# Performance work log

Hardware: AMD Instinct MI355X
Metric: run time of the kernel (lower is better)

Reference implementation:

```python
import jax, jax.numpy as jnp
import numpy as np


def setup_inputs() -> dict:
    key = jax.random.key(0)
    ks = jax.random.split(key, 5)
    B, T, E, C = 4, 1024, 4, 512
    IN, OUT = 2048, 8192
    return {
        "x": jax.random.normal(ks[0], (B, T, IN), dtype=jnp.float32),
        "combine_array": jax.random.uniform(ks[1], (B, T, E, C), dtype=jnp.float32),
        "dispatch_mask": jax.random.uniform(ks[2], (B, T, E, C), dtype=jnp.float32),
        "weight": jax.random.normal(ks[3], (OUT, IN), dtype=jnp.float32) * 0.02,
        "bias": jax.random.normal(ks[4], (OUT,), dtype=jnp.float32) * 0.02,
        "num_experts": E,
    }


def reference(x, combine_array, dispatch_mask, weight, bias, num_experts):
    E = num_experts
    i = weight.shape[1] // E  # expert_in_features
    w = weight.reshape(E, -1, i)  # (E, out, i) -- same reshape as torch
    B = x.shape[0]
    xr = x.reshape(B, -1, E, i)  # (B, T, E, i)
    # dispatch: gather tokens into expert capacity slots via dense mask
    xd = jnp.einsum('btei,btec->beci', xr, dispatch_mask)  # (B, E, C, i)
    # homogeneous coordinates to fold bias into the matmul (as in original)
    x_homo = jnp.concatenate([xd, jnp.ones_like(xd[..., :1])], axis=-1)  # (B,E,C,i+1)
    b_col = jnp.broadcast_to(bias.reshape(1, -1, 1), (E, w.shape[1], 1))
    w_homo = jnp.concatenate([w, b_col], axis=-1)  # (E, out, i+1)
    # per-expert matmul then combine back to tokens
    y = jnp.einsum('beci,eoi->beco', x_homo, w_homo)  # (B, E, C, out)
    return jnp.einsum('beco,btec->bto', y, combine_array)  # (B, T, out)
```

## Files before the change

### kernel.cpp

```cpp
#include <hip/hip_runtime.h>

#define B_   4
#define T_   1024
#define E_   4
#define C_   512
#define IN_  2048
#define OUT_ 8192
#define EI_  512

typedef float f32x4 __attribute__((ext_vector_type(4)));
typedef __bf16 bf16x8 __attribute__((ext_vector_type(8)));
typedef unsigned short ushort8 __attribute__((ext_vector_type(8)));

__device__ __forceinline__ unsigned short f32_bf16(float f) {
  unsigned int u = __float_as_uint(f);
  u += 0x7FFFu + ((u >> 16) & 1u);
  return (unsigned short)(u >> 16);
}

__device__ __forceinline__ void gl2lds16(const void* g, void* l) {
  __builtin_amdgcn_global_load_lds(
      (const __attribute__((address_space(1))) void*)g,
      (__attribute__((address_space(3))) void*)l, 16, 0, 0);
}

__global__ __launch_bounds__(256)
void prep(const float* __restrict__ xsrc, const float* __restrict__ msrc,
          const float* __restrict__ combine, const float* __restrict__ weight,
          unsigned short* __restrict__ xdst, unsigned short* __restrict__ mdst,
          unsigned short* __restrict__ comb_bf, float* __restrict__ S,
          unsigned short* __restrict__ W2) {
  const int bid = blockIdx.x;
  const int u = threadIdx.x;
  if (bid < 4096) {
    __shared__ float tile[64][65];
    const int z = bid >> 9;
    const int which = z >> 2;
    const int b = z & 3;
    const int rem = bid & 511;
    const int t0 = (rem >> 5) * 64;
    const int k0 = (rem & 31) * 64;
    const float* src = which ? msrc : xsrc;
    unsigned short* dst = which ? mdst : xdst;
    const int lrow = u >> 4;
    const int lcol = (u & 15) * 4;
    const float* s = src + (size_t)b * (T_ * 2048) + (size_t)t0 * 2048 + k0;
#pragma unroll
    for (int r = 0; r < 4; r++) {
      float4 v = *(const float4*)(s + (size_t)(lrow + 16 * r) * 2048 + lcol);
      tile[lrow + 16 * r][lcol]     = v.x;
      tile[lrow + 16 * r][lcol + 1] = v.y;
      tile[lrow + 16 * r][lcol + 2] = v.z;
      tile[lrow + 16 * r][lcol + 3] = v.w;
    }
    __syncthreads();
    const int kr = u >> 2;
    const int tq = (u & 3) * 8;
    const int kg = k0 + kr;
    const int e  = kg >> 9;
    const int kl = kg & 511;
    unsigned short* d = dst + (((size_t)b * 4 + e) * 512 + kl) * 1024 + t0 + tq;
#pragma unroll
    for (int s8 = 0; s8 < 2; s8++) {
      ushort8 rr;
#pragma unroll
      for (int j = 0; j < 8; j++) rr[j] = f32_bf16(tile[tq + s8 * 32 + j][kr]);
      *(ushort8*)(d + s8 * 32) = rr;
    }
  } else if (bid < 8192) {
    __shared__ float red[256];
    const int row = bid - 4096;
    const float4* p = (const float4*)(combine + (size_t)row * 2048) + (size_t)u * 2;
    float4 a = p[0], b = p[1];
    ushort8 r;
    r[0] = f32_bf16(a.x); r[1] = f32_bf16(a.y);
    r[2] = f32_bf16(a.z); r[3] = f32_bf16(a.w);
    r[4] = f32_bf16(b.x); r[5] = f32_bf16(b.y);
    r[6] = f32_bf16(b.z); r[7] = f32_bf16(b.w);
    *((ushort8*)(comb_bf + (size_t)row * 2048) + u) = r;
    float s = (a.x + a.y + a.z + a.w) + (b.x + b.y + b.z + b.w);
    red[u] = s;
    __syncthreads();
#pragma unroll
    for (int st = 128; st > 0; st >>= 1) {
      if (u < st) red[u] += red[u + st];
      __syncthreads();
    }
    if (u == 0) S[row] = red[0];
  } else {
    const int tid = (bid - 8192) * 256 + u;
    const int i8 = tid & 63;
    const int e  = (tid >> 6) & 3;
    const int o  = tid >> 8;
    const float* s = weight + (size_t)e * 4194304 + (size_t)o * 512 + i8 * 8;
    float4 a = *(const float4*)s;
    float4 b = *(const float4*)(s + 4);
    ushort8 r;
    r[0] = f32_bf16(a.x); r[1] = f32_bf16(a.y);
    r[2] = f32_bf16(a.z); r[3] = f32_bf16(a.w);
    r[4] = f32_bf16(b.x); r[5] = f32_bf16(b.y);
    r[6] = f32_bf16(b.z); r[7] = f32_bf16(b.w);
    *(ushort8*)(W2 + (size_t)o * 2048 + e * 512 + i8 * 8) = r;
  }
}

template <int MODE>
__global__ __launch_bounds__(256, 2)
void gemm_bt(const unsigned short* __restrict__ A,
             const unsigned short* __restrict__ Bm,
             void* __restrict__ Out, const float* __restrict__ bias,
             const float* __restrict__ S,
             int lda, int ldb, int ldo, int K, int Ediv,
             long sAb, long sAe, long sBb, long sBe, long sOb, long sOe) {
  __shared__ __align__(16) unsigned short As[2][4096];
  __shared__ __align__(16) unsigned short Bs[2][4096];
  const int u = threadIdx.x;
  const int z = blockIdx.z;
  const int zb = z / Ediv, ze = z % Ediv;
  const unsigned short* Ab = A  + zb * sAb + ze * sAe + (long)(blockIdx.y * 128) * lda;
  const unsigned short* Bb = Bm + zb * sBb + ze * sBe + (long)(blockIdx.x * 128) * ldb;

  const int srow = u >> 2;
  const int scol = (u & 3) * 8;
  const unsigned short* ga0 = Ab + (long)srow * lda + scol;
  const unsigned short* ga1 = ga0 + (long)64 * lda;
  const unsigned short* gb0 = Bb + (long)srow * ldb + scol;
  const unsigned short* gb1 = gb0 + (long)64 * ldb;

  const int w = u >> 6, lane = u & 63;
  const int wq = w * 512;

  const int wm = (w & 1) * 64, wn = (w >> 1) * 64;
  const int fm = lane & 15, fk = (lane >> 4) * 8;

  f32x4 acc[4][4] = {};

  gl2lds16(ga0, As[0] + wq);
  gl2lds16(ga1, As[0] + wq + 2048);
  gl2lds16(gb0, Bs[0] + wq);
  gl2lds16(gb1, Bs[0] + wq + 2048);
  ga0 += 32; ga1 += 32; gb0 += 32; gb1 += 32;
  __syncthreads();

  const int nt = K / 32;
  for (int t = 0; t < nt; ++t) {
    const int cur = t & 1;
    if (t + 1 < nt) {
      const int nx = cur ^ 1;
      gl2lds16(ga0, As[nx] + wq);
      gl2lds16(ga1, As[nx] + wq + 2048);
      gl2lds16(gb0, Bs[nx] + wq);
      gl2lds16(gb1, Bs[nx] + wq + 2048);
      ga0 += 32; ga1 += 32; gb0 += 32; gb1 += 32;
    }
    const unsigned short* pA = As[cur] + (wm + fm) * 32 + fk;
    const unsigned short* pB = Bs[cur] + (wn + fm) * 32 + fk;
    bf16x8 af[4], bfv[4];
#pragma unroll
    for (int i = 0; i < 4; i++) {
      af[i]  = *(const bf16x8*)(pA + i * 16 * 32);
      bfv[i] = *(const bf16x8*)(pB + i * 16 * 32);
    }
#pragma unroll
    for (int i = 0; i < 4; i++)
#pragma unroll
      for (int j = 0; j < 4; j++)
        acc[i][j] = __builtin_amdgcn_mfma_f32_16x16x32_bf16(af[i], bfv[j],
                                                            acc[i][j], 0, 0, 0);
    __syncthreads();
  }

  const long ob = zb * sOb + ze * sOe;
  const int em0 = blockIdx.y * 128 + wm + ((lane >> 4) << 2);
  const int en0 = blockIdx.x * 128 + wn + (lane & 15);
  float bcol[4];
  if (MODE == 1) {
#pragma unroll
    for (int j = 0; j < 4; j++) bcol[j] = bias[en0 + j * 16];
  }
#pragma unroll
  for (int i = 0; i < 4; i++)
#pragma unroll
    for (int r = 0; r < 4; r++) {
      const int m = em0 + i * 16 + r;
      const float sm = (MODE == 1) ? S[m] : 0.0f;
#pragma unroll
      for (int j = 0; j < 4; j++) {
        const long off = ob + (long)m * ldo + en0 + j * 16;
        if (MODE == 1)
          ((float*)Out)[off] = acc[i][j][r] + sm * bcol[j];
        else
          ((unsigned short*)Out)[off] = f32_bf16(acc[i][j][r]);
      }
    }
}

#define DSR(dst, addr) do { f32x4 _t_; \
    asm volatile("ds_read_b128 %0, %1" : "=v"(_t_) : "v"(addr)); \
    dst = __builtin_bit_cast(bf16x8, _t_); } while (0)

__global__ __launch_bounds__(512, 2)
void gemm256(const unsigned short* __restrict__ A,
             const unsigned short* __restrict__ Bm,
             float* __restrict__ Out,
             const float* __restrict__ bias,
             const float* __restrict__ S) {
  __shared__ __align__(16) unsigned short lds[65536];
  char* ldsg = (char*)lds;
  const unsigned ldsb =
      (unsigned)(unsigned long long)(__attribute__((address_space(3))) char*)(void*)lds;

  int wg = blockIdx.x;
  wg = (wg & 7) * 64 + (wg >> 3);
  const int bx = wg & 31;
  const int by = wg >> 5;

  const int u = threadIdx.x;
  const int w = u >> 6, lane = u & 63;
  const unsigned w1024 = (unsigned)(w * 1024);
  const int wmw = (w >> 2) * 128;
  const int wnw = (w & 3) * 64;
  const int fm = lane & 15;

  const unsigned hi16  = (unsigned)(((lane >> 4) & 3) * 16);
  const unsigned xorv  = (unsigned)((fm & 7) << 4);
  const unsigned colS0 = hi16 ^ xorv;
  const unsigned aR0 = (unsigned)((wmw + fm) * 128) + colS0;
  const unsigned aR1 = aR0 ^ 64u;
  const unsigned bR0 = 65536u + (unsigned)((wnw + fm) * 128) + colS0;
  const unsigned bR1 = bR0 ^ 64u;

  const int srr = w * 8 + (lane >> 3);
  const unsigned swzS = (unsigned)((((lane & 7) ^ ((lane >> 3) & 7)) << 4));
  const char* gA = (const char*)(A  + (size_t)(by * 256) * 2048) + (size_t)srr * 4096 + swzS;
  const char* gB = (const char*)(Bm + (size_t)(bx * 256) * 2048) + (size_t)srr * 4096 + swzS;

#define STG(gsrc, loff) do { \
    gl2lds16((gsrc), ldsg + (loff)); \
    gl2lds16((gsrc) + 262144, ldsg + (loff) + 8192); } while (0)

  STG(gA,                    0u + w1024);
  STG(gA + 524288,       16384u + w1024);
  STG(gB,                65536u + w1024);
  STG(gB + 524288,       81920u + w1024);
  STG(gA + 128,          32768u + w1024);
  STG(gA + 128 + 524288, 49152u + w1024);
  asm volatile("s_waitcnt vmcnt(4)" ::: "memory");
  __builtin_amdgcn_s_barrier();

  f32x4 acc[8][4] = {};
  bf16x8 a0[4][2], a1[4][2], bq[2][2];

  for (int kt = 0; kt < 32; ++kt) {
    const unsigned bbO = (unsigned)((kt & 1) * 32768);
    const unsigned nbR = bbO ^ 32768u;
    const int ktB = (kt + 1 < 32) ? kt + 1 : 31;
    const int ktA = (kt + 2 < 32) ? kt + 2 : 31;
    const char* gBn = gB + ktB * 128;
    const char* gAn = gA + ktA * 128;

#pragma unroll
    for (int i = 0; i < 4; ++i) {
      DSR(a0[i][0], ldsb + bbO + aR0 + (unsigned)(i * 2048));
      DSR(a0[i][1], ldsb + bbO + aR1 + (unsigned)(i * 2048));
    }
#pragma unroll
    for (int j = 0; j < 2; ++j) {
      DSR(bq[j][0], ldsb + bbO + bR0 + (unsigned)(j * 2048));
      DSR(bq[j][1], ldsb + bbO + bR1 + (unsigned)(j * 2048));
    }
    STG(gBn, 65536u + nbR + w1024);
    __builtin_amdgcn_s_barrier();
    asm volatile("s_waitcnt lgkmcnt(0)" ::: "memory");
    __builtin_amdgcn_sched_barrier(0);
    __builtin_amdgcn_s_setprio(1);
#pragma unroll
    for (int i = 0; i < 4; ++i)
#pragma unroll
      for (int j = 0; j < 2; ++j) {
        acc[i][j] = __builtin_amdgcn_mfma_f32_16x16x32_bf16(a0[i][0], bq[j][0], acc[i][j], 0, 0, 0);
        acc[i][j] = __builtin_amdgcn_mfma_f32_16x16x32_bf16(a0[i][1], bq[j][1], acc[i][j], 0, 0, 0);
      }
    __builtin_amdgcn_s_setprio(0);
    __builtin_amdgcn_s_barrier();

#pragma unroll
    for (int i = 0; i < 4; ++i) {
      DSR(a1[i][0], ldsb + bbO + aR0 + (unsigned)((4 + i) * 2048));
      DSR(a1[i][1], ldsb + bbO + aR1 + (unsigned)((4 + i) * 2048));
    }
    STG(gBn + 524288, 81920u + nbR + w1024);
    __builtin_amdgcn_s_barrier();
    asm volatile("s_waitcnt lgkmcnt(0)" ::: "memory");
    __builtin_amdgcn_sched_barrier(0);
    __builtin_amdgcn_s_setprio(1);
#pragma unroll
    for (int i = 0; i < 4; ++i)
#pragma unroll
      for (int j = 0; j < 2; ++j) {
        acc[4 + i][j] = __builtin_amdgcn_mfma_f32_16x16x32_bf16(a1[i][0], bq[j][0], acc[4 + i][j], 0, 0, 0);
        acc[4 + i][j] = __builtin_amdgcn_mfma_f32_16x16x32_bf16(a1[i][1], bq[j][1], acc[4 + i][j], 0, 0, 0);
      }
    __builtin_amdgcn_s_setprio(0);
    __builtin_amdgcn_s_barrier();

#pragma unroll
    for (int j = 0; j < 2; ++j) {
      DSR(bq[j][0], ldsb + bbO + bR0 + (unsigned)((2 + j) * 2048));
      DSR(bq[j][1], ldsb + bbO + bR1 + (unsigned)((2 + j) * 2048));
    }
    STG(gAn, bbO + w1024);
    __builtin_amdgcn_s_barrier();
    asm volatile("s_waitcnt lgkmcnt(0)" ::: "memory");
    __builtin_amdgcn_sched_barrier(0);
    __builtin_amdgcn_s_setprio(1);
#pragma unroll
    for (int i = 0; i < 4; ++i)
#pragma unroll
      for (int j = 0; j < 2; ++j) {
        acc[i][2 + j] = __builtin_amdgcn_mfma_f32_16x16x32_bf16(a0[i][0], bq[j][0], acc[i][2 + j], 0, 0, 0);
        acc[i][2 + j] = __builtin_amdgcn_mfma_f32_16x16x32_bf16(a0[i][1], bq[j][1], acc[i][2 + j], 0, 0, 0);
      }
    __builtin_amdgcn_s_setprio(0);
    __builtin_amdgcn_s_barrier();

    STG(gAn + 524288, bbO + 16384u + w1024);
    __builtin_amdgcn_s_barrier();
    __builtin_amdgcn_s_setprio(1);
#pragma unroll
    for (int i = 0; i < 4; ++i)
#pragma unroll
      for (int j = 0; j < 2; ++j) {
        acc[4 + i][2 + j] = __builtin_amdgcn_mfma_f32_16x16x32_bf16(a1[i][0], bq[j][0], acc[4 + i][2 + j], 0, 0, 0);
        acc[4 + i][2 + j] = __builtin_amdgcn_mfma_f32_16x16x32_bf16(a1[i][1], bq[j][1], acc[4 + i][2 + j], 0, 0, 0);
      }
    __builtin_amdgcn_s_setprio(0);
    asm volatile("s_waitcnt vmcnt(4)" ::: "memory");
    __builtin_amdgcn_sched_barrier(0);
    __builtin_amdgcn_s_barrier();
  }
#undef STG
  asm volatile("s_waitcnt vmcnt(0)" ::: "memory");

  const int m0 = by * 256 + wmw + ((lane >> 4) << 2);
  const int n0 = bx * 256 + wnw + (lane & 15);
  float bc[4];
#pragma unroll
  for (int j = 0; j < 4; ++j) bc[j] = bias[n0 + j * 16];
#pragma unroll
  for (int i = 0; i < 8; ++i)
#pragma unroll
    for (int r = 0; r < 4; ++r) {
      const int m = m0 + i * 16 + r;
      const float sm = S[m];
#pragma unroll
      for (int j = 0; j < 4; ++j)
        Out[(size_t)m * 8192 + n0 + j * 16] = acc[i][j][r] + sm * bc[j];
    }
}

extern "C" void kernel_launch(void* const* d_in, const int* in_sizes, int n_in,
                              void* d_out, int out_size, void* d_ws,
                              size_t ws_size, hipStream_t stream) {
  (void)in_sizes; (void)n_in; (void)out_size; (void)ws_size;
  const float* x       = (const float*)d_in[0];
  const float* combine = (const float*)d_in[1];
  const float* mask    = (const float*)d_in[2];
  const float* weight  = (const float*)d_in[3];
  const float* bias    = (const float*)d_in[4];
  float* out = (float*)d_out;

  char* ws = (char*)d_ws;
  unsigned short* W2      = (unsigned short*)ws;
  unsigned short* comb_bf = (unsigned short*)(ws + 33554432);
  float*          S       = (float*)(ws + 50331648);
  unsigned short* xT      = (unsigned short*)(ws + 51380224);
  unsigned short* maskT   = (unsigned short*)(ws + 68157440);
  unsigned short* xdT     = (unsigned short*)(ws + 84934656);
  unsigned short* zbuf    = (unsigned short*)(ws + 93323264);

  prep<<<16384, 256, 0, stream>>>(x, mask, combine, weight, xT, maskT,
                                  comb_bf, S, W2);

  gemm_bt<0><<<dim3(4, 4, 16), 256, 0, stream>>>(
      xT, maskT, (void*)xdT, nullptr, nullptr, 1024, 1024, 512, 1024,
      4, 2097152L, 524288L, 2097152L, 524288L, 1048576L, 262144L);

  gemm_bt<0><<<dim3(4, 8, 16), 256, 0, stream>>>(
      comb_bf, xdT, (void*)zbuf, nullptr, nullptr, 2048, 512, 2048, 512,
      4, 2097152L, 512L, 1048576L, 262144L, 2097152L, 512L);

  gemm256<<<dim3(512), 512, 0, stream>>>(zbuf, W2, out, bias, S);
}
```

Before: 415.3 us.

## Triple-buffer gemm_bt LDS pipeline with async waits and nontemporal output stores

Reworks the 128x128 gemm_bt kernel from a double-buffered loop with __syncthreads into a three-stage LDS ring. Loads are issued two tiles ahead, completion is tracked with explicit vmcnt/lgkmcnt waits and raw s_barrier, fragments are read with inline ds_read_b128, and wave priority is raised around the MFMA block. This is meant to hide global-load latency and cut barrier stalls. It raises LDS use to 48KB per block, which may limit occupancy, and it issues redundant clamped loads on the final iterations. The gemm256 epilogue also switches to nontemporal stores for the large fp32 output.

```diff
diff --git a/kernel.cpp b/kernel.cpp
--- a/kernel.cpp
+++ b/kernel.cpp
@@ -23,6 +23,10 @@
       (const __attribute__((address_space(1))) void*)g,
       (__attribute__((address_space(3))) void*)l, 16, 0, 0);
 }
+
+#define DSR(dst, addr) do { f32x4 _t_; \
+    asm volatile("ds_read_b128 %0, %1" : "=v"(_t_) : "v"(addr)); \
+    dst = __builtin_bit_cast(bf16x8, _t_); } while (0)
 
 __global__ __launch_bounds__(256)
 void prep(const float* __restrict__ xsrc, const float* __restrict__ msrc,
@@ -112,8 +116,11 @@
              const float* __restrict__ S,
              int lda, int ldb, int ldo, int K, int Ediv,
              long sAb, long sAe, long sBb, long sBe, long sOb, long sOe) {
-  __shared__ __align__(16) unsigned short As[2][4096];
-  __shared__ __align__(16) unsigned short Bs[2][4096];
+  __shared__ __align__(16) char ldsRaw[49152];
+  char* ldsg = ldsRaw;
+  const unsigned ldsb =
+      (unsigned)(unsigned long long)(__attribute__((address_space(3))) char*)(void*)ldsRaw;
+
   const int u = threadIdx.x;
   const int z = blockIdx.z;
   const int zb = z / Ediv, ze = z % Ediv;
@@ -122,53 +129,63 @@
 
   const int srow = u >> 2;
   const int scol = (u & 3) * 8;
-  const unsigned short* ga0 = Ab + (long)srow * lda + scol;
-  const unsigned short* ga1 = ga0 + (long)64 * lda;
-  const unsigned short* gb0 = Bb + (long)srow * ldb + scol;
-  const unsigned short* gb1 = gb0 + (long)64 * ldb;
+  const unsigned short* gA = Ab + (long)srow * lda + scol;
+  const unsigned short* gB = Bb + (long)srow * ldb + scol;
+  const long a64 = (long)64 * lda, b64 = (long)64 * ldb;
 
   const int w = u >> 6, lane = u & 63;
-  const int wq = w * 512;
+  const unsigned w1024 = (unsigned)(w * 1024);
 
   const int wm = (w & 1) * 64, wn = (w >> 1) * 64;
   const int fm = lane & 15, fk = (lane >> 4) * 8;
+  const unsigned aF = (unsigned)((wm + fm) * 64 + fk * 2);
+  const unsigned bF = 24576u + (unsigned)((wn + fm) * 64 + fk * 2);
 
   f32x4 acc[4][4] = {};
 
-  gl2lds16(ga0, As[0] + wq);
-  gl2lds16(ga1, As[0] + wq + 2048);
-  gl2lds16(gb0, Bs[0] + wq);
-  gl2lds16(gb1, Bs[0] + wq + 2048);
-  ga0 += 32; ga1 += 32; gb0 += 32; gb1 += 32;
-  __syncthreads();
-
   const int nt = K / 32;
+#define STGBT(buf, kk) do { \
+    const unsigned short* a_ = gA + (kk) * 32; \
+    const unsigned short* b_ = gB + (kk) * 32; \
+    gl2lds16(a_,       ldsg + (buf) * 8192 + w1024); \
+    gl2lds16(a_ + a64, ldsg + (buf) * 8192 + 4096 + w1024); \
+    gl2lds16(b_,       ldsg + 24576 + (buf) * 8192 + w1024); \
+    gl2lds16(b_ + b64, ldsg + 24576 + (buf) * 8192 + 4096 + w1024); } while (0)
+
+  STGBT(0, 0);
+  STGBT(1, 1);
+  asm volatile("s_waitcnt vmcnt(4)" ::: "memory");
+  __builtin_amdgcn_s_barrier();
+
+  int cur = 0, pre = 2;
   for (int t = 0; t < nt; ++t) {
-    const int cur = t & 1;
-    if (t + 1 < nt) {
-      const int nx = cur ^ 1;
-      gl2lds16(ga0, As[nx] + wq);
-      gl2lds16(ga1, As[nx] + wq + 2048);
-      gl2lds16(gb0, Bs[nx] + wq);
-      gl2lds16(gb1, Bs[nx] + wq + 2048);
-      ga0 += 32; ga1 += 32; gb0 += 32; gb1 += 32;
-    }
-    const unsigned short* pA = As[cur] + (wm + fm) * 32 + fk;
-    const unsigned short* pB = Bs[cur] + (wn + fm) * 32 + fk;
     bf16x8 af[4], bfv[4];
+    const unsigned cb = (unsigned)(cur * 8192);
 #pragma unroll
     for (int i = 0; i < 4; i++) {
-      af[i]  = *(const bf16x8*)(pA + i * 16 * 32);
-      bfv[i] = *(const bf16x8*)(pB + i * 16 * 32);
-    }
+      DSR(af[i],  ldsb + cb + aF + (unsigned)(i * 1024));
+      DSR(bfv[i], ldsb + cb + bF + (unsigned)(i * 1024));
+    }
+    const int kk = (t + 2 < nt) ? t + 2 : nt - 1;
+    STGBT(pre, kk);
+    asm volatile("s_waitcnt lgkmcnt(0)" ::: "memory");
+    __builtin_amdgcn_sched_barrier(0);
+    __builtin_amdgcn_s_setprio(1);
 #pragma unroll
     for (int i = 0; i < 4; i++)
 #pragma unroll
       for (int j = 0; j < 4; j++)
         acc[i][j] = __builtin_amdgcn_mfma_f32_16x16x32_bf16(af[i], bfv[j],
                                                             acc[i][j], 0, 0, 0);
-    __syncthreads();
+    __builtin_amdgcn_s_setprio(0);
+    asm volatile("s_waitcnt vmcnt(4)" ::: "memory");
+    __builtin_amdgcn_sched_barrier(0);
+    __builtin_amdgcn_s_barrier();
+    cur = (cur == 2) ? 0 : cur + 1;
+    pre = (pre == 2) ? 0 : pre + 1;
   }
+#undef STGBT
+  asm volatile("s_waitcnt vmcnt(0)" ::: "memory");
 
   const long ob = zb * sOb + ze * sOe;
   const int em0 = blockIdx.y * 128 + wm + ((lane >> 4) << 2);
@@ -194,10 +211,6 @@
       }
     }
 }
-
-#define DSR(dst, addr) do { f32x4 _t_; \
-    asm volatile("ds_read_b128 %0, %1" : "=v"(_t_) : "v"(addr)); \
-    dst = __builtin_bit_cast(bf16x8, _t_); } while (0)
 
 __global__ __launch_bounds__(512, 2)
 void gemm256(const unsigned short* __restrict__ A,
@@ -355,7 +368,8 @@
       const float sm = S[m];
 #pragma unroll
       for (int j = 0; j < 4; ++j)
-        Out[(size_t)m * 8192 + n0 + j * 16] = acc[i][j][r] + sm * bc[j];
+        __builtin_nontemporal_store(acc[i][j][r] + sm * bc[j],
+                                    &Out[(size_t)m * 8192 + n0 + j * 16]);
     }
 }
 
```

New measurement: 414.9 us. About the same (-0.1%).
